# Kernel tuning notes

Measured on AMD Instinct MI355X. Metric: run time of the kernel, lower is better.

Reference implementation:

```python
import jax, jax.numpy as jnp
import numpy as np

N_NODES = 100000
N_EDGES = 1600000
NODE_DIM = 64
EDGE_DIM = 32
HIDDEN = 64


def setup_inputs() -> dict:
    key = jax.random.key(0)
    ks = jax.random.split(key, 12)

    def lin(k, out_d, in_d):
        # torch Linear default init: U(-1/sqrt(in), 1/sqrt(in))
        bound = 1.0 / np.sqrt(in_d)
        kw, kb = jax.random.split(k)
        W = jax.random.uniform(kw, (out_d, in_d), jnp.float32, -bound, bound)
        b = jax.random.uniform(kb, (out_d,), jnp.float32, -bound, bound)
        return W, b

    x = jax.random.normal(ks[0], (N_NODES, NODE_DIM), jnp.float32)
    edge_index = jax.random.randint(ks[1], (2, N_EDGES), 0, N_NODES, jnp.int64)
    edge_feat = jax.random.normal(ks[2], (N_EDGES, EDGE_DIM), jnp.float32)

    We1, be1 = lin(ks[3], HIDDEN, NODE_DIM * 2 + EDGE_DIM)
    We2, be2 = lin(ks[4], HIDDEN, HIDDEN)
    Wn1, bn1 = lin(ks[5], HIDDEN, NODE_DIM + HIDDEN)
    Wn2, bn2 = lin(ks[6], HIDDEN, HIDDEN)

    return {
        "x": x, "edge_index": edge_index, "edge_feat": edge_feat,
        "We1": We1, "be1": be1, "We2": We2, "be2": be2,
        "Wn1": Wn1, "bn1": bn1, "Wn2": Wn2, "bn2": bn2,
    }


def reference(x, edge_index, edge_feat, We1, be1, We2, be2, Wn1, bn1, Wn2, bn2):
    row, col = edge_index[0], edge_index[1]
    # gather endpoint features and concat with edge features: [E, 2*node+edge]
    m_input = jnp.concatenate([x[row], x[col], edge_feat], axis=-1)
    # edge MLP: Linear -> SiLU -> Linear -> SiLU
    h = jax.nn.silu(m_input @ We1.T + be1)
    m_ij = jax.nn.silu(h @ We2.T + be2)
    # scatter_add over source nodes (row), dim_size = N
    agg = jax.ops.segment_sum(m_ij, row, num_segments=x.shape[0])
    # node MLP: Linear -> SiLU -> Linear
    h2 = jax.nn.silu(jnp.concatenate([x, agg], axis=-1) @ Wn1.T + bn1)
    return h2 @ Wn2.T + bn2
```

## Files before the change

kernel.cpp:

```cpp
#include <hip/hip_runtime.h>

#define N_NODES 100000
#define N_EDGES 1600000

typedef short s8v __attribute__((ext_vector_type(8)));
typedef float f4v __attribute__((ext_vector_type(4)));
typedef unsigned short us4 __attribute__((ext_vector_type(4)));

__device__ inline unsigned short f2bf(float f) {
    unsigned int u = __float_as_uint(f);
    u += 0x7FFFu + ((u >> 16) & 1u);
    return (unsigned short)(u >> 16);
}

__device__ inline float silu_f(float v) {
    return v / (1.0f + __expf(-v));
}

__global__ __launch_bounds__(256) void x2bf_kernel(const float* __restrict__ x,
                                                   unsigned short* __restrict__ xb)
{
    const int total = N_NODES * 64 / 4;
    for (int i = blockIdx.x * blockDim.x + threadIdx.x; i < total;
         i += gridDim.x * blockDim.x) {
        f4v v = *(const f4v*)(x + (size_t)i * 4);
        us4 o;
        #pragma unroll
        for (int q = 0; q < 4; ++q) o[q] = f2bf(v[q]);
        *(us4*)(xb + (size_t)i * 4) = o;
    }
}

__global__ __launch_bounds__(256, 4) void edge_kernel(
    const unsigned short* __restrict__ xb, const int* __restrict__ eidx,
    const float* __restrict__ ef,
    const float* __restrict__ We1, const float* __restrict__ be1,
    const float* __restrict__ We2, const float* __restrict__ be2,
    float* agg)
{
    __shared__ unsigned short W1L[64 * 160];
    __shared__ unsigned short W2L[64 * 64];
    __shared__ unsigned short HL[4][2][64][8];

    const int tid = threadIdx.x;

    for (int i = tid; i < 64 * 160; i += 256) {
        int row = i / 160;
        int k   = i - row * 160;
        int t = row >> 4, lr = row & 15;
        int s = k >> 5, kg = (k >> 3) & 3, j = k & 7;
        W1L[(((t * 5 + s) * 64) + (kg * 16 + lr)) * 8 + j] = f2bf(We1[i]);
    }
    for (int i = tid; i < 64 * 64; i += 256) {
        int row = i >> 6;
        int k   = i & 63;
        int t = row >> 4, lr = row & 15;
        int s = k >> 5, kg = (k >> 3) & 3, j = k & 7;
        W2L[(((t * 2 + s) * 64) + (kg * 16 + lr)) * 8 + j] = f2bf(We2[i]);
    }
    __syncthreads();

    const int lane = tid & 63;
    const int wv   = tid >> 6;
    const int lrow = lane & 15;
    const int lkg  = lane >> 4;

    float b1f[4], b2f[4];
    #pragma unroll
    for (int t = 0; t < 4; ++t) {
        b1f[t] = be1[t * 16 + lrow];
        b2f[t] = be2[t * 16 + lrow];
    }

    const int n_groups = N_EDGES / 16;
    const int wave_id  = blockIdx.x * 4 + wv;
    const int n_waves  = gridDim.x * 4;

    for (int grp = wave_id; grp < n_groups; grp += n_waves) {
        const int e0 = grp * 16;

        const int r = eidx[e0 + lrow];
        const int c = eidx[N_EDGES + e0 + lrow];

        s8v afr[5];
        afr[0] = *(const s8v*)(xb + (size_t)r * 64 + lkg * 8);
        afr[1] = *(const s8v*)(xb + (size_t)r * 64 + 32 + lkg * 8);
        afr[2] = *(const s8v*)(xb + (size_t)c * 64 + lkg * 8);
        afr[3] = *(const s8v*)(xb + (size_t)c * 64 + 32 + lkg * 8);
        {
            const float* ep = ef + (size_t)(e0 + lrow) * 32 + lkg * 8;
            f4v elo = *(const f4v*)ep;
            f4v ehi = *(const f4v*)(ep + 4);
            s8v a4;
            #pragma unroll
            for (int q = 0; q < 4; ++q) {
                a4[q]     = (short)f2bf(elo[q]);
                a4[q + 4] = (short)f2bf(ehi[q]);
            }
            afr[4] = a4;
        }

        f4v acc[4] = {f4v(0), f4v(0), f4v(0), f4v(0)};
        #pragma unroll
        for (int s = 0; s < 5; ++s) {
            #pragma unroll
            for (int t = 0; t < 4; ++t) {
                s8v b = *(const s8v*)&W1L[((t * 5 + s) * 64 + lane) * 8];
                acc[t] = __builtin_amdgcn_mfma_f32_16x16x32_bf16(afr[s], b, acc[t], 0, 0, 0);
            }
        }

        #pragma unroll
        for (int t = 0; t < 4; ++t) {
            const int col = t * 16 + lrow;
            const int s   = col >> 5;
            const int lsub = (col & 31) >> 3;
            const int j   = col & 7;
            #pragma unroll
            for (int rr = 0; rr < 4; ++rr) {
                float v = silu_f(acc[t][rr] + b1f[t]);
                HL[wv][s][lsub * 16 + (lkg * 4 + rr)][j] = f2bf(v);
            }
        }

        s8v h0 = *(const s8v*)&HL[wv][0][lane][0];
        s8v h1 = *(const s8v*)&HL[wv][1][lane][0];
        f4v c2[4] = {f4v(0), f4v(0), f4v(0), f4v(0)};
        #pragma unroll
        for (int t = 0; t < 4; ++t) {
            s8v b0 = *(const s8v*)&W2L[((t * 2 + 0) * 64 + lane) * 8];
            s8v b1 = *(const s8v*)&W2L[((t * 2 + 1) * 64 + lane) * 8];
            c2[t] = __builtin_amdgcn_mfma_f32_16x16x32_bf16(h0, b0, c2[t], 0, 0, 0);
            c2[t] = __builtin_amdgcn_mfma_f32_16x16x32_bf16(h1, b1, c2[t], 0, 0, 0);
        }

        #pragma unroll
        for (int rr = 0; rr < 4; ++rr) {
            const int node = __shfl(r, lkg * 4 + rr);
            float* dst = agg + (size_t)node * 64;
            #pragma unroll
            for (int t = 0; t < 4; ++t) {
                float v = silu_f(c2[t][rr] + b2f[t]);
                atomicAdd(dst + t * 16 + lrow, v);
            }
        }
    }
}

__global__ __launch_bounds__(256) void node_kernel(
    const float* __restrict__ x,
    const float* __restrict__ Wn1, const float* __restrict__ bn1,
    const float* __restrict__ Wn2, const float* __restrict__ bn2,
    float* io)
{
    __shared__ unsigned short A[64][136];
    __shared__ unsigned short W1[64][136];
    __shared__ unsigned short H[64][72];
    __shared__ unsigned short W2[64][72];
    __shared__ float B1[64];
    __shared__ float B2[64];

    const int tid = threadIdx.x;

    for (int i = tid; i < 64 * 128; i += 256) {
        W1[i >> 7][i & 127] = f2bf(Wn1[i]);
    }
    for (int i = tid; i < 64 * 64; i += 256) {
        W2[i >> 6][i & 63] = f2bf(Wn2[i]);
    }
    if (tid < 64) { B1[tid] = bn1[tid]; B2[tid] = bn2[tid]; }

    const int n0  = blockIdx.x * 64;
    const int g   = tid >> 4;
    const int l16 = tid & 15;
    #pragma unroll
    for (int i = 0; i < 4; ++i) {
        int e = g + i * 16;
        int n = n0 + e;
        if (n >= N_NODES) n = N_NODES - 1;

        f4v xv = *(const f4v*)(x + (size_t)n * 64 + l16 * 4);
        us4 av;
        #pragma unroll
        for (int q = 0; q < 4; ++q) av[q] = f2bf(xv[q]);
        *(us4*)&A[e][l16 * 4] = av;

        f4v gv = *(const f4v*)(io + (size_t)n * 64 + l16 * 4);
        us4 ag;
        #pragma unroll
        for (int q = 0; q < 4; ++q) ag[q] = f2bf(gv[q]);
        *(us4*)&A[e][64 + l16 * 4] = ag;
    }
    __syncthreads();

    const int lane = tid & 63;
    const int m0   = (tid >> 6) * 16;
    const int lrow = lane & 15;
    const int lkg  = lane >> 4;

    f4v acc0 = 0, acc1 = 0, acc2 = 0, acc3 = 0;
    #pragma unroll
    for (int s = 0; s < 4; ++s) {
        int k0 = s * 32 + lkg * 8;
        s8v a = *(const s8v*)&A[m0 + lrow][k0];
        s8v b0 = *(const s8v*)&W1[ 0 + lrow][k0];
        s8v b1 = *(const s8v*)&W1[16 + lrow][k0];
        s8v b2 = *(const s8v*)&W1[32 + lrow][k0];
        s8v b3 = *(const s8v*)&W1[48 + lrow][k0];
        acc0 = __builtin_amdgcn_mfma_f32_16x16x32_bf16(a, b0, acc0, 0, 0, 0);
        acc1 = __builtin_amdgcn_mfma_f32_16x16x32_bf16(a, b1, acc1, 0, 0, 0);
        acc2 = __builtin_amdgcn_mfma_f32_16x16x32_bf16(a, b2, acc2, 0, 0, 0);
        acc3 = __builtin_amdgcn_mfma_f32_16x16x32_bf16(a, b3, acc3, 0, 0, 0);
    }
    {
        f4v accs[4] = {acc0, acc1, acc2, acc3};
        #pragma unroll
        for (int t = 0; t < 4; ++t) {
            int col = t * 16 + lrow;
            float bias = B1[col];
            #pragma unroll
            for (int r = 0; r < 4; ++r) {
                float v = silu_f(accs[t][r] + bias);
                H[m0 + lkg * 4 + r][col] = f2bf(v);
            }
        }
    }

    f4v c0 = 0, c1 = 0, c2 = 0, c3 = 0;
    #pragma unroll
    for (int s = 0; s < 2; ++s) {
        int k0 = s * 32 + lkg * 8;
        s8v a = *(const s8v*)&H[m0 + lrow][k0];
        s8v b0 = *(const s8v*)&W2[ 0 + lrow][k0];
        s8v b1 = *(const s8v*)&W2[16 + lrow][k0];
        s8v b2 = *(const s8v*)&W2[32 + lrow][k0];
        s8v b3 = *(const s8v*)&W2[48 + lrow][k0];
        c0 = __builtin_amdgcn_mfma_f32_16x16x32_bf16(a, b0, c0, 0, 0, 0);
        c1 = __builtin_amdgcn_mfma_f32_16x16x32_bf16(a, b1, c1, 0, 0, 0);
        c2 = __builtin_amdgcn_mfma_f32_16x16x32_bf16(a, b2, c2, 0, 0, 0);
        c3 = __builtin_amdgcn_mfma_f32_16x16x32_bf16(a, b3, c3, 0, 0, 0);
    }
    {
        f4v cs[4] = {c0, c1, c2, c3};
        #pragma unroll
        for (int r = 0; r < 4; ++r) {
            int n = n0 + m0 + lkg * 4 + r;
            if (n < N_NODES) {
                float* dst = io + (size_t)n * 64;
                #pragma unroll
                for (int t = 0; t < 4; ++t) {
                    int col = t * 16 + lrow;
                    dst[col] = cs[t][r] + B2[col];
                }
            }
        }
    }
}

extern "C" void kernel_launch(void* const* d_in, const int* in_sizes, int n_in,
                              void* d_out, int out_size, void* d_ws, size_t ws_size,
                              hipStream_t stream) {
    const float* x    = (const float*)d_in[0];
    const int*   eidx = (const int*)  d_in[1];
    const float* ef   = (const float*)d_in[2];
    const float* We1  = (const float*)d_in[3];
    const float* be1  = (const float*)d_in[4];
    const float* We2  = (const float*)d_in[5];
    const float* be2  = (const float*)d_in[6];
    const float* Wn1  = (const float*)d_in[7];
    const float* bn1  = (const float*)d_in[8];
    const float* Wn2  = (const float*)d_in[9];
    const float* bn2  = (const float*)d_in[10];
    float* out = (float*)d_out;

    unsigned short* xb = (unsigned short*)d_ws;

    hipMemsetAsync(d_out, 0, (size_t)N_NODES * 64 * sizeof(float), stream);

    x2bf_kernel<<<1024, 256, 0, stream>>>(x, xb);
    edge_kernel<<<1024, 256, 0, stream>>>(xb, eidx, ef, We1, be1, We2, be2, out);
    node_kernel<<<(N_NODES + 63) / 64, 256, 0, stream>>>(x, Wn1, bn1, Wn2, bn2, out);
}
```

Baseline: 458.3 us.

## Sort edges by source node and fuse edge MLP, aggregation and node MLP

```diff
diff --git a/kernel.cpp b/kernel.cpp
--- a/kernel.cpp
+++ b/kernel.cpp
@@ -31,7 +31,278 @@
     }
 }
 
-__global__ __launch_bounds__(256, 4) void edge_kernel(
+__global__ __launch_bounds__(256) void hist_kernel(const int* __restrict__ eidx,
+                                                   int* cnt)
+{
+    for (int e = blockIdx.x * blockDim.x + threadIdx.x; e < N_EDGES;
+         e += gridDim.x * blockDim.x)
+        atomicAdd(&cnt[eidx[e]], 1);
+}
+
+#define SCAN_NBLK 98
+
+__global__ __launch_bounds__(1024) void scanA_kernel(const int* __restrict__ cnt,
+                                                     int* base, int* bsum)
+{
+    __shared__ int sh[1024];
+    const int t = threadIdx.x;
+    const int i = blockIdx.x * 1024 + t;
+    int c = (i < N_NODES) ? cnt[i] : 0;
+    sh[t] = c;
+    __syncthreads();
+    for (int off = 1; off < 1024; off <<= 1) {
+        int v = (t >= off) ? sh[t - off] : 0;
+        __syncthreads();
+        sh[t] += v;
+        __syncthreads();
+    }
+    if (i < N_NODES) base[i] = sh[t];
+    if (t == 1023) bsum[blockIdx.x] = sh[1023];
+}
+
+__global__ __launch_bounds__(128) void scanB_kernel(const int* __restrict__ bsum,
+                                                    int* boff)
+{
+    __shared__ int sh[128];
+    const int t = threadIdx.x;
+    int v = (t < SCAN_NBLK) ? bsum[t] : 0;
+    sh[t] = v;
+    __syncthreads();
+    for (int off = 1; off < 128; off <<= 1) {
+        int u = (t >= off) ? sh[t - off] : 0;
+        __syncthreads();
+        sh[t] += u;
+        __syncthreads();
+    }
+    boff[t] = sh[t] - v;
+}
+
+__global__ __launch_bounds__(256) void scanC_kernel(const int* __restrict__ cnt,
+                                                    int* base, const int* __restrict__ boff,
+                                                    int* cur)
+{
+    const int i = blockIdx.x * 256 + threadIdx.x;
+    if (i < N_NODES) {
+        int b = base[i] - cnt[i] + boff[i >> 10];
+        base[i] = b;
+        cur[i]  = b;
+    }
+}
+
+__global__ __launch_bounds__(256) void perm_kernel(const int* __restrict__ eidx,
+                                                   int* cur, int2* __restrict__ elist)
+{
+    for (int e = blockIdx.x * blockDim.x + threadIdx.x; e < N_EDGES;
+         e += gridDim.x * blockDim.x) {
+        int r = eidx[e];
+        int c = eidx[N_EDGES + e];
+        int pos = atomicAdd(&cur[r], 1);
+        elist[pos] = make_int2(e | ((r & 63) << 25), c);
+    }
+}
+
+__global__ __launch_bounds__(512, 4) void fused_kernel(
+    const unsigned short* __restrict__ xb, const float* __restrict__ ef,
+    const int* __restrict__ base, const int2* __restrict__ elist,
+    const float* __restrict__ We1, const float* __restrict__ be1,
+    const float* __restrict__ We2, const float* __restrict__ be2,
+    const float* __restrict__ Wn1, const float* __restrict__ bn1,
+    const float* __restrict__ Wn2, const float* __restrict__ bn2,
+    float* __restrict__ out)
+{
+    __shared__ unsigned short W1L[64 * 160];
+    __shared__ unsigned short W2L[64 * 64];
+    __shared__ unsigned short HL[8][2][64][8];
+    __shared__ float AGG[65][64];
+
+    const int tid = threadIdx.x;
+
+    for (int i = tid; i < 64 * 160; i += 512) {
+        int row = i / 160, k = i - row * 160;
+        int t = row >> 4, lr = row & 15, s = k >> 5, kg = (k >> 3) & 3, j = k & 7;
+        W1L[(((t * 5 + s) * 64) + (kg * 16 + lr)) * 8 + j] = f2bf(We1[i]);
+    }
+    for (int i = tid; i < 64 * 64; i += 512) {
+        int row = i >> 6, k = i & 63;
+        int t = row >> 4, lr = row & 15, s = k >> 5, kg = (k >> 3) & 3, j = k & 7;
+        W2L[(((t * 2 + s) * 64) + (kg * 16 + lr)) * 8 + j] = f2bf(We2[i]);
+    }
+    for (int i = tid; i < 65 * 64; i += 512) ((float*)AGG)[i] = 0.0f;
+    __syncthreads();
+
+    const int lane = tid & 63;
+    const int wv   = tid >> 6;
+    const int lrow = lane & 15;
+    const int lkg  = lane >> 4;
+
+    const int n0    = blockIdx.x * 64;
+    const int base0 = base[n0];
+    const int end   = (n0 + 64 <= N_NODES) ? base[n0 + 64] : N_EDGES;
+
+    float b1f[4], b2f[4];
+    #pragma unroll
+    for (int t = 0; t < 4; ++t) {
+        b1f[t] = be1[t * 16 + lrow];
+        b2f[t] = be2[t * 16 + lrow];
+    }
+
+    for (int t0 = base0 + wv * 16; t0 < end; t0 += 8 * 16) {
+        const int  idx   = t0 + lrow;
+        const bool valid = idx < end;
+        int2 ent = elist[valid ? idx : base0];
+        const int e     = ent.x & 0x1FFFFFF;
+        const int ar    = valid ? (ent.x >> 25) : 64;
+        const int c     = ent.y;
+        const int rowid = n0 + (ent.x >> 25);
+
+        s8v afr[5];
+        afr[0] = *(const s8v*)(xb + (size_t)rowid * 64 + lkg * 8);
+        afr[1] = *(const s8v*)(xb + (size_t)rowid * 64 + 32 + lkg * 8);
+        afr[2] = *(const s8v*)(xb + (size_t)c * 64 + lkg * 8);
+        afr[3] = *(const s8v*)(xb + (size_t)c * 64 + 32 + lkg * 8);
+        {
+            const float* ep = ef + (size_t)e * 32 + lkg * 8;
+            f4v elo = *(const f4v*)ep;
+            f4v ehi = *(const f4v*)(ep + 4);
+            s8v a4;
+            #pragma unroll
+            for (int q = 0; q < 4; ++q) {
+                a4[q]     = (short)f2bf(elo[q]);
+                a4[q + 4] = (short)f2bf(ehi[q]);
+            }
+            afr[4] = a4;
+        }
+
+        f4v acc[4] = {f4v(0), f4v(0), f4v(0), f4v(0)};
+        #pragma unroll
+        for (int s = 0; s < 5; ++s) {
+            #pragma unroll
+            for (int t = 0; t < 4; ++t) {
+                s8v b = *(const s8v*)&W1L[((t * 5 + s) * 64 + lane) * 8];
+                acc[t] = __builtin_amdgcn_mfma_f32_16x16x32_bf16(afr[s], b, acc[t], 0, 0, 0);
+            }
+        }
+
+        #pragma unroll
+        for (int t = 0; t < 4; ++t) {
+            const int col = t * 16 + lrow;
+            const int s = col >> 5, lsub = (col & 31) >> 3, j = col & 7;
+            #pragma unroll
+            for (int rr = 0; rr < 4; ++rr) {
+                float v = silu_f(acc[t][rr] + b1f[t]);
+                HL[wv][s][lsub * 16 + (lkg * 4 + rr)][j] = f2bf(v);
+            }
+        }
+
+        s8v h0 = *(const s8v*)&HL[wv][0][lane][0];
+        s8v h1 = *(const s8v*)&HL[wv][1][lane][0];
+        f4v c2[4] = {f4v(0), f4v(0), f4v(0), f4v(0)};
+        #pragma unroll
+        for (int t = 0; t < 4; ++t) {
+            s8v b0 = *(const s8v*)&W2L[((t * 2 + 0) * 64 + lane) * 8];
+            s8v b1 = *(const s8v*)&W2L[((t * 2 + 1) * 64 + lane) * 8];
+            c2[t] = __builtin_amdgcn_mfma_f32_16x16x32_bf16(h0, b0, c2[t], 0, 0, 0);
+            c2[t] = __builtin_amdgcn_mfma_f32_16x16x32_bf16(h1, b1, c2[t], 0, 0, 0);
+        }
+
+        #pragma unroll
+        for (int rr = 0; rr < 4; ++rr) {
+            const int arb = __shfl(ar, lkg * 4 + rr);
+            #pragma unroll
+            for (int t = 0; t < 4; ++t) {
+                float v = silu_f(c2[t][rr] + b2f[t]);
+                atomicAdd(&AGG[arb][t * 16 + lrow], v);
+            }
+        }
+    }
+    __syncthreads();
+
+    for (int i = tid; i < 64 * 128; i += 512) {
+        int row = i >> 7, k = i & 127;
+        int t = row >> 4, lr = row & 15, s = k >> 5, kg = (k >> 3) & 3, j = k & 7;
+        W1L[(((t * 4 + s) * 64) + (kg * 16 + lr)) * 8 + j] = f2bf(Wn1[i]);
+    }
+    for (int i = tid; i < 64 * 64; i += 512) {
+        int row = i >> 6, k = i & 63;
+        int t = row >> 4, lr = row & 15, s = k >> 5, kg = (k >> 3) & 3, j = k & 7;
+        W2L[(((t * 2 + s) * 64) + (kg * 16 + lr)) * 8 + j] = f2bf(Wn2[i]);
+    }
+    __syncthreads();
+
+    if (wv < 4) {
+        const int m0 = wv * 16;
+        float n1f[4], n2f[4];
+        #pragma unroll
+        for (int t = 0; t < 4; ++t) {
+            n1f[t] = bn1[t * 16 + lrow];
+            n2f[t] = bn2[t * 16 + lrow];
+        }
+
+        const int n  = n0 + m0 + lrow;
+        const int nc = (n < N_NODES) ? n : (N_NODES - 1);
+
+        s8v a[4];
+        a[0] = *(const s8v*)(xb + (size_t)nc * 64 + lkg * 8);
+        a[1] = *(const s8v*)(xb + (size_t)nc * 64 + 32 + lkg * 8);
+        #pragma unroll
+        for (int s = 0; s < 2; ++s) {
+            f4v g0 = *(const f4v*)&AGG[m0 + lrow][s * 32 + lkg * 8];
+            f4v g1 = *(const f4v*)&AGG[m0 + lrow][s * 32 + lkg * 8 + 4];
+            s8v av;
+            #pragma unroll
+            for (int q = 0; q < 4; ++q) {
+                av[q]     = (short)f2bf(g0[q]);
+                av[q + 4] = (short)f2bf(g1[q]);
+            }
+            a[2 + s] = av;
+        }
+
+        f4v acc[4] = {f4v(0), f4v(0), f4v(0), f4v(0)};
+        #pragma unroll
+        for (int s = 0; s < 4; ++s) {
+            #pragma unroll
+            for (int t = 0; t < 4; ++t) {
+                s8v b = *(const s8v*)&W1L[((t * 4 + s) * 64 + lane) * 8];
+                acc[t] = __builtin_amdgcn_mfma_f32_16x16x32_bf16(a[s], b, acc[t], 0, 0, 0);
+            }
+        }
+
+        #pragma unroll
+        for (int t = 0; t < 4; ++t) {
+            const int col = t * 16 + lrow;
+            const int s = col >> 5, lsub = (col & 31) >> 3, j = col & 7;
+            #pragma unroll
+            for (int rr = 0; rr < 4; ++rr) {
+                float v = silu_f(acc[t][rr] + n1f[t]);
+                HL[wv][s][lsub * 16 + (lkg * 4 + rr)][j] = f2bf(v);
+            }
+        }
+
+        s8v h0 = *(const s8v*)&HL[wv][0][lane][0];
+        s8v h1 = *(const s8v*)&HL[wv][1][lane][0];
+        f4v c2[4] = {f4v(0), f4v(0), f4v(0), f4v(0)};
+        #pragma unroll
+        for (int t = 0; t < 4; ++t) {
+            s8v b0 = *(const s8v*)&W2L[((t * 2 + 0) * 64 + lane) * 8];
+            s8v b1 = *(const s8v*)&W2L[((t * 2 + 1) * 64 + lane) * 8];
+            c2[t] = __builtin_amdgcn_mfma_f32_16x16x32_bf16(h0, b0, c2[t], 0, 0, 0);
+            c2[t] = __builtin_amdgcn_mfma_f32_16x16x32_bf16(h1, b1, c2[t], 0, 0, 0);
+        }
+
+        #pragma unroll
+        for (int rr = 0; rr < 4; ++rr) {
+            const int nrow = n0 + m0 + lkg * 4 + rr;
+            if (nrow < N_NODES) {
+                float* dst = out + (size_t)nrow * 64;
+                #pragma unroll
+                for (int t = 0; t < 4; ++t)
+                    dst[t * 16 + lrow] = c2[t][rr] + n2f[t];
+            }
+        }
+    }
+}
+
+__global__ __launch_bounds__(256, 4) void edge_kernel_fb(
     const unsigned short* __restrict__ xb, const int* __restrict__ eidx,
     const float* __restrict__ ef,
     const float* __restrict__ We1, const float* __restrict__ be1,
@@ -43,45 +314,28 @@
     __shared__ unsigned short HL[4][2][64][8];
 
     const int tid = threadIdx.x;
-
     for (int i = tid; i < 64 * 160; i += 256) {
-        int row = i / 160;
-        int k   = i - row * 160;
-        int t = row >> 4, lr = row & 15;
-        int s = k >> 5, kg = (k >> 3) & 3, j = k & 7;
+        int row = i / 160, k = i - row * 160;
+        int t = row >> 4, lr = row & 15, s = k >> 5, kg = (k >> 3) & 3, j = k & 7;
         W1L[(((t * 5 + s) * 64) + (kg * 16 + lr)) * 8 + j] = f2bf(We1[i]);
     }
     for (int i = tid; i < 64 * 64; i += 256) {
-        int row = i >> 6;
-        int k   = i & 63;
-        int t = row >> 4, lr = row & 15;
-        int s = k >> 5, kg = (k >> 3) & 3, j = k & 7;
+        int row = i >> 6, k = i & 63;
+        int t = row >> 4, lr = row & 15, s = k >> 5, kg = (k >> 3) & 3, j = k & 7;
         W2L[(((t * 2 + s) * 64) + (kg * 16 + lr)) * 8 + j] = f2bf(We2[i]);
     }
     __syncthreads();
 
-    const int lane = tid & 63;
-    const int wv   = tid >> 6;
-    const int lrow = lane & 15;
-    const int lkg  = lane >> 4;
-
+    const int lane = tid & 63, wv = tid >> 6, lrow = lane & 15, lkg = lane >> 4;
     float b1f[4], b2f[4];
     #pragma unroll
-    for (int t = 0; t < 4; ++t) {
-        b1f[t] = be1[t * 16 + lrow];
-        b2f[t] = be2[t * 16 + lrow];
-    }
-
-    const int n_groups = N_EDGES / 16;
-    const int wave_id  = blockIdx.x * 4 + wv;
-    const int n_waves  = gridDim.x * 4;
-
-    for (int grp = wave_id; grp < n_groups; grp += n_waves) {
+    for (int t = 0; t < 4; ++t) { b1f[t] = be1[t*16+lrow]; b2f[t] = be2[t*16+lrow]; }
+
+    const int wave_id = blockIdx.x * 4 + wv, n_waves = gridDim.x * 4;
+    for (int grp = wave_id; grp < N_EDGES / 16; grp += n_waves) {
         const int e0 = grp * 16;
-
         const int r = eidx[e0 + lrow];
         const int c = eidx[N_EDGES + e0 + lrow];
-
         s8v afr[5];
         afr[0] = *(const s8v*)(xb + (size_t)r * 64 + lkg * 8);
         afr[1] = *(const s8v*)(xb + (size_t)r * 64 + 32 + lkg * 8);
@@ -89,65 +343,49 @@
         afr[3] = *(const s8v*)(xb + (size_t)c * 64 + 32 + lkg * 8);
         {
             const float* ep = ef + (size_t)(e0 + lrow) * 32 + lkg * 8;
-            f4v elo = *(const f4v*)ep;
-            f4v ehi = *(const f4v*)(ep + 4);
+            f4v elo = *(const f4v*)ep, ehi = *(const f4v*)(ep + 4);
             s8v a4;
             #pragma unroll
-            for (int q = 0; q < 4; ++q) {
-                a4[q]     = (short)f2bf(elo[q]);
-                a4[q + 4] = (short)f2bf(ehi[q]);
-            }
+            for (int q = 0; q < 4; ++q) { a4[q] = (short)f2bf(elo[q]); a4[q+4] = (short)f2bf(ehi[q]); }
             afr[4] = a4;
         }
-
         f4v acc[4] = {f4v(0), f4v(0), f4v(0), f4v(0)};
         #pragma unroll
-        for (int s = 0; s < 5; ++s) {
+        for (int s = 0; s < 5; ++s)
             #pragma unroll
             for (int t = 0; t < 4; ++t) {
                 s8v b = *(const s8v*)&W1L[((t * 5 + s) * 64 + lane) * 8];
                 acc[t] = __builtin_amdgcn_mfma_f32_16x16x32_bf16(afr[s], b, acc[t], 0, 0, 0);
             }
-        }
-
-        #pragma unroll
-        for (int t = 0; t < 4; ++t) {
-            const int col = t * 16 + lrow;
-            const int s   = col >> 5;
-            const int lsub = (col & 31) >> 3;
-            const int j   = col & 7;
-            #pragma unroll
-            for (int rr = 0; rr < 4; ++rr) {
-                float v = silu_f(acc[t][rr] + b1f[t]);
-                HL[wv][s][lsub * 16 + (lkg * 4 + rr)][j] = f2bf(v);
-            }
-        }
-
+        #pragma unroll
+        for (int t = 0; t < 4; ++t) {
+            const int col = t*16+lrow, s = col >> 5, lsub = (col & 31) >> 3, j = col & 7;
+            #pragma unroll
+            for (int rr = 0; rr < 4; ++rr)
+                HL[wv][s][lsub*16 + (lkg*4+rr)][j] = f2bf(silu_f(acc[t][rr] + b1f[t]));
+        }
         s8v h0 = *(const s8v*)&HL[wv][0][lane][0];
         s8v h1 = *(const s8v*)&HL[wv][1][lane][0];
         f4v c2[4] = {f4v(0), f4v(0), f4v(0), f4v(0)};
         #pragma unroll
         for (int t = 0; t < 4; ++t) {
-            s8v b0 = *(const s8v*)&W2L[((t * 2 + 0) * 64 + lane) * 8];
-            s8v b1 = *(const s8v*)&W2L[((t * 2 + 1) * 64 + lane) * 8];
+            s8v b0 = *(const s8v*)&W2L[((t*2+0)*64+lane)*8];
+            s8v b1 = *(const s8v*)&W2L[((t*2+1)*64+lane)*8];
             c2[t] = __builtin_amdgcn_mfma_f32_16x16x32_bf16(h0, b0, c2[t], 0, 0, 0);
             c2[t] = __builtin_amdgcn_mfma_f32_16x16x32_bf16(h1, b1, c2[t], 0, 0, 0);
         }
-
         #pragma unroll
         for (int rr = 0; rr < 4; ++rr) {
             const int node = __shfl(r, lkg * 4 + rr);
             float* dst = agg + (size_t)node * 64;
             #pragma unroll
-            for (int t = 0; t < 4; ++t) {
-                float v = silu_f(c2[t][rr] + b2f[t]);
-                atomicAdd(dst + t * 16 + lrow, v);
-            }
-        }
-    }
-}
-
-__global__ __launch_bounds__(256) void node_kernel(
+            for (int t = 0; t < 4; ++t)
+                atomicAdd(dst + t * 16 + lrow, silu_f(c2[t][rr] + b2f[t]));
+        }
+    }
+}
+
+__global__ __launch_bounds__(256) void node_kernel_fb(
     const float* __restrict__ x,
     const float* __restrict__ Wn1, const float* __restrict__ bn1,
     const float* __restrict__ Wn2, const float* __restrict__ bn2,
@@ -161,30 +399,20 @@
     __shared__ float B2[64];
 
     const int tid = threadIdx.x;
-
-    for (int i = tid; i < 64 * 128; i += 256) {
-        W1[i >> 7][i & 127] = f2bf(Wn1[i]);
-    }
-    for (int i = tid; i < 64 * 64; i += 256) {
-        W2[i >> 6][i & 63] = f2bf(Wn2[i]);
-    }
+    for (int i = tid; i < 64 * 128; i += 256) W1[i >> 7][i & 127] = f2bf(Wn1[i]);
+    for (int i = tid; i < 64 * 64; i += 256) W2[i >> 6][i & 63] = f2bf(Wn2[i]);
     if (tid < 64) { B1[tid] = bn1[tid]; B2[tid] = bn2[tid]; }
 
-    const int n0  = blockIdx.x * 64;
-    const int g   = tid >> 4;
-    const int l16 = tid & 15;
+    const int n0 = blockIdx.x * 64, g = tid >> 4, l16 = tid & 15;
     #pragma unroll
     for (int i = 0; i < 4; ++i) {
-        int e = g + i * 16;
-        int n = n0 + e;
+        int e = g + i * 16, n = n0 + e;
         if (n >= N_NODES) n = N_NODES - 1;
-
         f4v xv = *(const f4v*)(x + (size_t)n * 64 + l16 * 4);
         us4 av;
         #pragma unroll
         for (int q = 0; q < 4; ++q) av[q] = f2bf(xv[q]);
         *(us4*)&A[e][l16 * 4] = av;
-
         f4v gv = *(const f4v*)(io + (size_t)n * 64 + l16 * 4);
         us4 ag;
         #pragma unroll
@@ -193,52 +421,37 @@
     }
     __syncthreads();
 
-    const int lane = tid & 63;
-    const int m0   = (tid >> 6) * 16;
-    const int lrow = lane & 15;
-    const int lkg  = lane >> 4;
-
-    f4v acc0 = 0, acc1 = 0, acc2 = 0, acc3 = 0;
+    const int lane = tid & 63, m0 = (tid >> 6) * 16, lrow = lane & 15, lkg = lane >> 4;
+    f4v a0 = 0, a1 = 0, a2 = 0, a3 = 0;
     #pragma unroll
     for (int s = 0; s < 4; ++s) {
         int k0 = s * 32 + lkg * 8;
-        s8v a = *(const s8v*)&A[m0 + lrow][k0];
-        s8v b0 = *(const s8v*)&W1[ 0 + lrow][k0];
-        s8v b1 = *(const s8v*)&W1[16 + lrow][k0];
-        s8v b2 = *(const s8v*)&W1[32 + lrow][k0];
-        s8v b3 = *(const s8v*)&W1[48 + lrow][k0];
-        acc0 = __builtin_amdgcn_mfma_f32_16x16x32_bf16(a, b0, acc0, 0, 0, 0);
-        acc1 = __builtin_amdgcn_mfma_f32_16x16x32_bf16(a, b1, acc1, 0, 0, 0);
-        acc2 = __builtin_amdgcn_mfma_f32_16x16x32_bf16(a, b2, acc2, 0, 0, 0);
-        acc3 = __builtin_amdgcn_mfma_f32_16x16x32_bf16(a, b3, acc3, 0, 0, 0);
+        s8v av = *(const s8v*)&A[m0 + lrow][k0];
+        a0 = __builtin_amdgcn_mfma_f32_16x16x32_bf16(av, *(const s8v*)&W1[ 0+lrow][k0], a0, 0, 0, 0);
+        a1 = __builtin_amdgcn_mfma_f32_16x16x32_bf16(av, *(const s8v*)&W1[16+lrow][k0], a1, 0, 0, 0);
+        a2 = __builtin_amdgcn_mfma_f32_16x16x32_bf16(av, *(const s8v*)&W1[32+lrow][k0], a2, 0, 0, 0);
+        a3 = __builtin_amdgcn_mfma_f32_16x16x32_bf16(av, *(const s8v*)&W1[48+lrow][k0], a3, 0, 0, 0);
     }
     {
-        f4v accs[4] = {acc0, acc1, acc2, acc3};
+        f4v accs[4] = {a0, a1, a2, a3};
         #pragma unroll
         for (int t = 0; t < 4; ++t) {
             int col = t * 16 + lrow;
             float bias = B1[col];
             #pragma unroll
-            for (int r = 0; r < 4; ++r) {
-                float v = silu_f(accs[t][r] + bias);
-                H[m0 + lkg * 4 + r][col] = f2bf(v);
-            }
-        }
-    }
-
+            for (int r = 0; r < 4; ++r)
+                H[m0 + lkg * 4 + r][col] = f2bf(silu_f(accs[t][r] + bias));
+        }
+    }
     f4v c0 = 0, c1 = 0, c2 = 0, c3 = 0;
     #pragma unroll
     for (int s = 0; s < 2; ++s) {
         int k0 = s * 32 + lkg * 8;
-        s8v a = *(const s8v*)&H[m0 + lrow][k0];
-        s8v b0 = *(const s8v*)&W2[ 0 + lrow][k0];
-        s8v b1 = *(const s8v*)&W2[16 + lrow][k0];
-        s8v b2 = *(const s8v*)&W2[32 + lrow][k0];
-        s8v b3 = *(const s8v*)&W2[48 + lrow][k0];
-        c0 = __builtin_amdgcn_mfma_f32_16x16x32_bf16(a, b0, c0, 0, 0, 0);
-        c1 = __builtin_amdgcn_mfma_f32_16x16x32_bf16(a, b1, c1, 0, 0, 0);
-        c2 = __builtin_amdgcn_mfma_f32_16x16x32_bf16(a, b2, c2, 0, 0, 0);
-        c3 = __builtin_amdgcn_mfma_f32_16x16x32_bf16(a, b3, c3, 0, 0, 0);
+        s8v av = *(const s8v*)&H[m0 + lrow][k0];
+        c0 = __builtin_amdgcn_mfma_f32_16x16x32_bf16(av, *(const s8v*)&W2[ 0+lrow][k0], c0, 0, 0, 0);
+        c1 = __builtin_amdgcn_mfma_f32_16x16x32_bf16(av, *(const s8v*)&W2[16+lrow][k0], c1, 0, 0, 0);
+        c2 = __builtin_amdgcn_mfma_f32_16x16x32_bf16(av, *(const s8v*)&W2[32+lrow][k0], c2, 0, 0, 0);
+        c3 = __builtin_amdgcn_mfma_f32_16x16x32_bf16(av, *(const s8v*)&W2[48+lrow][k0], c3, 0, 0, 0);
     }
     {
         f4v cs[4] = {c0, c1, c2, c3};
@@ -248,10 +461,7 @@
             if (n < N_NODES) {
                 float* dst = io + (size_t)n * 64;
                 #pragma unroll
-                for (int t = 0; t < 4; ++t) {
-                    int col = t * 16 + lrow;
-                    dst[col] = cs[t][r] + B2[col];
-                }
+                for (int t = 0; t < 4; ++t) dst[t * 16 + lrow] = cs[t][r] + B2[t * 16 + lrow];
             }
         }
     }
@@ -273,11 +483,30 @@
     const float* bn2  = (const float*)d_in[10];
     float* out = (float*)d_out;
 
-    unsigned short* xb = (unsigned short*)d_ws;
-
-    hipMemsetAsync(d_out, 0, (size_t)N_NODES * 64 * sizeof(float), stream);
+    char* ws = (char*)d_ws;
+    unsigned short* xb = (unsigned short*)ws;
+    int*  cnt   = (int*) (ws + 12800000);
+    int*  basep = (int*) (ws + 13200000);
+    int*  cur   = (int*) (ws + 13600000);
+    int*  bsum  = (int*) (ws + 14000000);
+    int*  boff  = (int*) (ws + 14000512);
+    int2* elist = (int2*)(ws + 14001024);
+    const size_t WS_NEEDED = 26801024;
 
     x2bf_kernel<<<1024, 256, 0, stream>>>(x, xb);
-    edge_kernel<<<1024, 256, 0, stream>>>(xb, eidx, ef, We1, be1, We2, be2, out);
-    node_kernel<<<(N_NODES + 63) / 64, 256, 0, stream>>>(x, Wn1, bn1, Wn2, bn2, out);
-}
+
+    if (ws_size >= WS_NEEDED) {
+        hipMemsetAsync(cnt, 0, N_NODES * sizeof(int), stream);
+        hist_kernel<<<2048, 256, 0, stream>>>(eidx, cnt);
+        scanA_kernel<<<SCAN_NBLK, 1024, 0, stream>>>(cnt, basep, bsum);
+        scanB_kernel<<<1, 128, 0, stream>>>(bsum, boff);
+        scanC_kernel<<<(N_NODES + 255) / 256, 256, 0, stream>>>(cnt, basep, boff, cur);
+        perm_kernel<<<2048, 256, 0, stream>>>(eidx, cur, elist);
+        fused_kernel<<<(N_NODES + 63) / 64, 512, 0, stream>>>(
+            xb, ef, basep, elist, We1, be1, We2, be2, Wn1, bn1, Wn2, bn2, out);
+    } else {
+        hipMemsetAsync(d_out, 0, (size_t)N_NODES * 64 * sizeof(float), stream);
+        edge_kernel_fb<<<1024, 256, 0, stream>>>(xb, eidx, ef, We1, be1, We2, be2, out);
+        node_kernel_fb<<<(N_NODES + 63) / 64, 256, 0, stream>>>(x, Wn1, bn1, Wn2, bn2, out);
+    }
+}
```

After: 836.1 us. 82.4% more time.
